# Kernel tuning notes

Hardware: AMD Instinct MI355X
Metric: run time of the kernel (lower is better)

The kernel has to match this reference:

```python
import jax, jax.numpy as jnp
import numpy as np


def setup_inputs() -> dict:
    key = jax.random.key(0)
    kx, ky = jax.random.split(key)
    n, m, d = 2048, 2048, 16  # d == n_wires
    x = jax.random.normal(kx, (n, d), dtype=jnp.float32)
    y = jax.random.normal(ky, (m, d), dtype=jnp.float32)
    return {"x": x, "y": y}


def reference(x, y):
    # RY gates on distinct wires commute; RY(-y_k) RY(x_k) = RY(x_k - y_k).
    # State = tensor product over wires of RY(x_k - y_k)|0>, so the |0...0>
    # amplitude is prod_k cos((x_k - y_k)/2). Original code stores abs(amplitude).
    half_diff = 0.5 * (x[:, None, :] - y[None, :, :])  # [n, m, d]
    kernel = jnp.abs(jnp.prod(jnp.cos(half_diff), axis=-1))  # [n, m]
    return kernel
```

## Files before the change

kernel.cpp:

```cpp
#include <hip/hip_runtime.h>
#include <hip/hip_bf16.h>


constexpr int D = 16;

typedef short  bf16x8 __attribute__((ext_vector_type(8)));
typedef float  f32x16 __attribute__((ext_vector_type(16)));

__device__ __align__(16) unsigned short Atab[64 * 2048];
__device__ __align__(16) unsigned short Btab[64 * 2048];

static __device__ inline unsigned int pk2(float a, float b) {
    __hip_bfloat16 ha = __float2bfloat16(a);
    __hip_bfloat16 hb = __float2bfloat16(b);
    unsigned short ua, ub;
    __builtin_memcpy(&ua, &ha, 2);
    __builtin_memcpy(&ub, &hb, 2);
    return (unsigned int)ua | ((unsigned int)ub << 16);
}

__global__ __launch_bounds__(256)
void qfact(const float* __restrict__ x, const float* __restrict__ y, int n) {
    const int tid  = blockIdx.x * 256 + threadIdx.x;
    const int u    = tid >> 1;
    const int half = tid & 1;
    const bool isrow = (u < n);
    const int  v   = isrow ? u : u - n;
    const float* src = (isrow ? x : y) + (size_t)v * D;
    unsigned short* tab = isrow ? Atab : Btab;
    const float scale = isrow ? 0.5f : 1.0f;

    float e[8];
    *(float4*)(e)     = *(const float4*)(src + 8 * half);
    *(float4*)(e + 4) = *(const float4*)(src + 8 * half + 4);

    float f[4][4];
#pragma unroll
    for (int pp = 0; pp < 4; ++pp) {
        const float a0 = e[2 * pp], a1 = e[2 * pp + 1];
        float sm, cm, sp, cp;
        __sincosf(0.5f * (a0 - a1), &sm, &cm);
        __sincosf(0.5f * (a0 + a1), &sp, &cp);
        f[pp][0] = scale * cm; f[pp][1] = scale * sm;
        f[pp][2] = scale * cp; f[pp][3] = scale * sp;
    }

    unsigned short* dst = tab + (size_t)(v >> 5) * 2048 + (size_t)(v & 31) * 8;
#pragma unroll
    for (int qq = 0; qq < 2; ++qq) {
        const int q = half * 2 + qq;
        const float* fa = f[2 * qq];
        const float* fb = f[2 * qq + 1];
        uint4 lo, hi;
        lo.x = pk2(fa[0] * fb[0], fa[0] * fb[1]);
        lo.y = pk2(fa[0] * fb[2], fa[0] * fb[3]);
        lo.z = pk2(fa[1] * fb[0], fa[1] * fb[1]);
        lo.w = pk2(fa[1] * fb[2], fa[1] * fb[3]);
        hi.x = pk2(fa[2] * fb[0], fa[2] * fb[1]);
        hi.y = pk2(fa[2] * fb[2], fa[2] * fb[3]);
        hi.z = pk2(fa[3] * fb[0], fa[3] * fb[1]);
        hi.w = pk2(fa[3] * fb[2], fa[3] * fb[3]);
        *(uint4*)(dst + (size_t)(q * 2 + 0) * 256) = lo;
        *(uint4*)(dst + (size_t)(q * 2 + 1) * 256) = hi;
    }
}

__global__ __launch_bounds__(256)
void qmain(float* __restrict__ out, int m) {
    const int wave = threadIdx.x >> 6;
    const int lane = threadIdx.x & 63;
    const int l31  = lane & 31;
    const int kh   = lane >> 5;
    const int rb   = blockIdx.x * 2 + (wave >> 1);
    const int cb   = blockIdx.y * 2 + (wave & 1);

    const unsigned short* abase = Atab + (size_t)rb * 2048 + (size_t)kh * 256 + (size_t)l31 * 8;
    const unsigned short* bbase = Btab + (size_t)cb * 2048 + (size_t)kh * 256 + (size_t)l31 * 8;

    bf16x8 a0 = *(const bf16x8*)(abase);
    bf16x8 b0 = *(const bf16x8*)(bbase);
    bf16x8 a1 = *(const bf16x8*)(abase + 512);
    bf16x8 b1 = *(const bf16x8*)(bbase + 512);
    bf16x8 a2 = *(const bf16x8*)(abase + 1024);
    bf16x8 b2 = *(const bf16x8*)(bbase + 1024);
    bf16x8 a3 = *(const bf16x8*)(abase + 1536);
    bf16x8 b3 = *(const bf16x8*)(bbase + 1536);

    const f32x16 zc = {0.f};
    f32x16 q0 = __builtin_amdgcn_mfma_f32_32x32x16_bf16(a0, b0, zc, 0, 0, 0);
    f32x16 q1 = __builtin_amdgcn_mfma_f32_32x32x16_bf16(a1, b1, zc, 0, 0, 0);
    f32x16 q2 = __builtin_amdgcn_mfma_f32_32x32x16_bf16(a2, b2, zc, 0, 0, 0);
    f32x16 q3 = __builtin_amdgcn_mfma_f32_32x32x16_bf16(a3, b3, zc, 0, 0, 0);
    const f32x16 prod = (q0 * q1) * (q2 * q3);

    const int ocol = cb * 32 + l31;
    float* base = out + (size_t)(rb * 32 + 4 * kh) * m + ocol;
#pragma unroll
    for (int r = 0; r < 16; ++r) {
        const int row_off = (r & 3) + 8 * (r >> 2);
        __builtin_nontemporal_store(fabsf(prod[r]), base + (size_t)row_off * m);
    }
}

extern "C" void kernel_launch(void* const* d_in, const int* in_sizes, int n_in,
                              void* d_out, int out_size, void* d_ws, size_t ws_size,
                              hipStream_t stream) {
    const float* x = (const float*)d_in[0];
    const float* y = (const float*)d_in[1];
    float* out = (float*)d_out;
    const int n = in_sizes[0] / D;
    const int m = in_sizes[1] / D;

    const int nvec = n + m;
    qfact<<<dim3((nvec * 2) / 256), 256, 0, stream>>>(x, y, n);

    dim3 grid(n / 64, m / 64);
    qmain<<<grid, 256, 0, stream>>>(out, m);
}
```

Baseline: 62.50 us.

## Fuse factor-table precompute into main kernel, building MFMA fragments in registers

Drops the separate precompute kernel and its global bf16 tables. Each wave now loads raw x/y rows and computes sincos products directly into MFMA operand fragments. This saves a kernel launch and a global-memory round trip. The cost is redundant trig work: each row vector is recomputed by many blocks (n/64 or m/64 times), and every lane computes all 8 pairs.

Result: no change. 62.70 us (+0.3%).

```diff
diff --git a/kernel.cpp b/kernel.cpp
--- a/kernel.cpp
+++ b/kernel.cpp
@@ -6,9 +6,6 @@
 
 typedef short  bf16x8 __attribute__((ext_vector_type(8)));
 typedef float  f32x16 __attribute__((ext_vector_type(16)));
-
-__device__ __align__(16) unsigned short Atab[64 * 2048];
-__device__ __align__(16) unsigned short Btab[64 * 2048];
 
 static __device__ inline unsigned int pk2(float a, float b) {
     __hip_bfloat16 ha = __float2bfloat16(a);
@@ -19,24 +16,30 @@
     return (unsigned int)ua | ((unsigned int)ub << 16);
 }
 
-__global__ __launch_bounds__(256)
-void qfact(const float* __restrict__ x, const float* __restrict__ y, int n) {
-    const int tid  = blockIdx.x * 256 + threadIdx.x;
-    const int u    = tid >> 1;
-    const int half = tid & 1;
-    const bool isrow = (u < n);
-    const int  v   = isrow ? u : u - n;
-    const float* src = (isrow ? x : y) + (size_t)v * D;
-    unsigned short* tab = isrow ? Atab : Btab;
-    const float scale = isrow ? 0.5f : 1.0f;
+static __device__ inline bf16x8 mkfrag(const float* fa, const float* fb, int kh) {
+    const float a0 = kh ? fa[2] : fa[0];
+    const float a1 = kh ? fa[3] : fa[1];
+    unsigned int w[4];
+    w[0] = pk2(a0 * fb[0], a0 * fb[1]);
+    w[1] = pk2(a0 * fb[2], a0 * fb[3]);
+    w[2] = pk2(a1 * fb[0], a1 * fb[1]);
+    w[3] = pk2(a1 * fb[2], a1 * fb[3]);
+    bf16x8 r;
+    __builtin_memcpy(&r, w, 16);
+    return r;
+}
 
-    float e[8];
-    *(float4*)(e)     = *(const float4*)(src + 8 * half);
-    *(float4*)(e + 4) = *(const float4*)(src + 8 * half + 4);
+static __device__ inline void mkside(const float* __restrict__ src, float scale,
+                                     int kh, bf16x8 frag[4]) {
+    float e[16];
+    *(float4*)(e + 0)  = *(const float4*)(src + 0);
+    *(float4*)(e + 4)  = *(const float4*)(src + 4);
+    *(float4*)(e + 8)  = *(const float4*)(src + 8);
+    *(float4*)(e + 12) = *(const float4*)(src + 12);
 
-    float f[4][4];
+    float f[8][4];
 #pragma unroll
-    for (int pp = 0; pp < 4; ++pp) {
+    for (int pp = 0; pp < 8; ++pp) {
         const float a0 = e[2 * pp], a1 = e[2 * pp + 1];
         float sm, cm, sp, cp;
         __sincosf(0.5f * (a0 - a1), &sm, &cm);
@@ -44,29 +47,14 @@
         f[pp][0] = scale * cm; f[pp][1] = scale * sm;
         f[pp][2] = scale * cp; f[pp][3] = scale * sp;
     }
-
-    unsigned short* dst = tab + (size_t)(v >> 5) * 2048 + (size_t)(v & 31) * 8;
 #pragma unroll
-    for (int qq = 0; qq < 2; ++qq) {
-        const int q = half * 2 + qq;
-        const float* fa = f[2 * qq];
-        const float* fb = f[2 * qq + 1];
-        uint4 lo, hi;
-        lo.x = pk2(fa[0] * fb[0], fa[0] * fb[1]);
-        lo.y = pk2(fa[0] * fb[2], fa[0] * fb[3]);
-        lo.z = pk2(fa[1] * fb[0], fa[1] * fb[1]);
-        lo.w = pk2(fa[1] * fb[2], fa[1] * fb[3]);
-        hi.x = pk2(fa[2] * fb[0], fa[2] * fb[1]);
-        hi.y = pk2(fa[2] * fb[2], fa[2] * fb[3]);
-        hi.z = pk2(fa[3] * fb[0], fa[3] * fb[1]);
-        hi.w = pk2(fa[3] * fb[2], fa[3] * fb[3]);
-        *(uint4*)(dst + (size_t)(q * 2 + 0) * 256) = lo;
-        *(uint4*)(dst + (size_t)(q * 2 + 1) * 256) = hi;
-    }
+    for (int q = 0; q < 4; ++q)
+        frag[q] = mkfrag(f[2 * q], f[2 * q + 1], kh);
 }
 
 __global__ __launch_bounds__(256)
-void qmain(float* __restrict__ out, int m) {
+void qkern(const float* __restrict__ x, const float* __restrict__ y,
+           float* __restrict__ out, int m) {
     const int wave = threadIdx.x >> 6;
     const int lane = threadIdx.x & 63;
     const int l31  = lane & 31;
@@ -74,23 +62,15 @@
     const int rb   = blockIdx.x * 2 + (wave >> 1);
     const int cb   = blockIdx.y * 2 + (wave & 1);
 
-    const unsigned short* abase = Atab + (size_t)rb * 2048 + (size_t)kh * 256 + (size_t)l31 * 8;
-    const unsigned short* bbase = Btab + (size_t)cb * 2048 + (size_t)kh * 256 + (size_t)l31 * 8;
-
-    bf16x8 a0 = *(const bf16x8*)(abase);
-    bf16x8 b0 = *(const bf16x8*)(bbase);
-    bf16x8 a1 = *(const bf16x8*)(abase + 512);
-    bf16x8 b1 = *(const bf16x8*)(bbase + 512);
-    bf16x8 a2 = *(const bf16x8*)(abase + 1024);
-    bf16x8 b2 = *(const bf16x8*)(bbase + 1024);
-    bf16x8 a3 = *(const bf16x8*)(abase + 1536);
-    bf16x8 b3 = *(const bf16x8*)(bbase + 1536);
+    bf16x8 a[4], b[4];
+    mkside(x + (size_t)(rb * 32 + l31) * D, 0.5f, kh, a);
+    mkside(y + (size_t)(cb * 32 + l31) * D, 1.0f, kh, b);
 
     const f32x16 zc = {0.f};
-    f32x16 q0 = __builtin_amdgcn_mfma_f32_32x32x16_bf16(a0, b0, zc, 0, 0, 0);
-    f32x16 q1 = __builtin_amdgcn_mfma_f32_32x32x16_bf16(a1, b1, zc, 0, 0, 0);
-    f32x16 q2 = __builtin_amdgcn_mfma_f32_32x32x16_bf16(a2, b2, zc, 0, 0, 0);
-    f32x16 q3 = __builtin_amdgcn_mfma_f32_32x32x16_bf16(a3, b3, zc, 0, 0, 0);
+    f32x16 q0 = __builtin_amdgcn_mfma_f32_32x32x16_bf16(a[0], b[0], zc, 0, 0, 0);
+    f32x16 q1 = __builtin_amdgcn_mfma_f32_32x32x16_bf16(a[1], b[1], zc, 0, 0, 0);
+    f32x16 q2 = __builtin_amdgcn_mfma_f32_32x32x16_bf16(a[2], b[2], zc, 0, 0, 0);
+    f32x16 q3 = __builtin_amdgcn_mfma_f32_32x32x16_bf16(a[3], b[3], zc, 0, 0, 0);
     const f32x16 prod = (q0 * q1) * (q2 * q3);
 
     const int ocol = cb * 32 + l31;
@@ -111,9 +91,6 @@
     const int n = in_sizes[0] / D;
     const int m = in_sizes[1] / D;
 
-    const int nvec = n + m;
-    qfact<<<dim3((nvec * 2) / 256), 256, 0, stream>>>(x, y, n);
-
     dim3 grid(n / 64, m / 64);
-    qmain<<<grid, 256, 0, stream>>>(out, m);
+    qkern<<<grid, 256, 0, stream>>>(x, y, out, m);
 }
```
